# Performance work log

Measured on AMD Instinct MI355X. Metric: run time of the kernel, lower is better.

## Reference

```python
import jax, jax.numpy as jnp
import numpy as np

C = 768; NH = 12; HD = C // NH; P = 16; IMG = 256; HS = IMG // P  # 16x16 patch grid
WIN = 7; HWP = WIN // 2  # half window (pad)
DEPTH = 12; MLP = 4 * C
B = 32; T = 1
OFFS = [(dh, dw) for dh in range(WIN) for dw in range(WIN)]


def ln(x, g, b, eps=1e-5):
    mu = jnp.mean(x, axis=-1, keepdims=True)
    var = jnp.mean((x - mu) ** 2, axis=-1, keepdims=True)
    return (x - mu) * jax.lax.rsqrt(var + eps) * g + b


def local_attn(x, qkv_w, proj_w, proj_b):
    # x: (B, N, C) with N = HS*HS (T=1); sliding-window attention, zero-padded keys
    Bc, N, _ = x.shape
    qkv = (x @ qkv_w.T).reshape(Bc, N, 3, NH, HD)
    q, k, v = [jnp.transpose(qkv[:, :, i], (0, 2, 1, 3)).reshape(Bc, NH, HS, HS, HD)
               for i in range(3)]
    scale = HD ** -0.5
    kp = jnp.pad(k, ((0, 0), (0, 0), (HWP, HWP), (HWP, HWP), (0, 0)))
    vp = jnp.pad(v, ((0, 0), (0, 0), (HWP, HWP), (HWP, HWP), (0, 0)))
    # per-offset logits; padded (zero) keys give logit 0, matching torch's zero-pad softmax
    scores = jnp.stack([
        jnp.einsum('bnhwd,bnhwd->bnhw', q, kp[:, :, dh:dh + HS, dw:dw + HS]) * scale
        for dh, dw in OFFS], axis=-1)  # (B, NH, HS, HS, 49)
    attn = jax.nn.softmax(scores, axis=-1)
    out = sum(attn[..., i, None] * vp[:, :, dh:dh + HS, dw:dw + HS]
              for i, (dh, dw) in enumerate(OFFS))  # (B, NH, HS, HS, HD)
    out = jnp.transpose(out, (0, 2, 3, 1, 4)).reshape(Bc, N, C)
    return out @ proj_w.T + proj_b


def global_attn(x, in_w, in_b, out_w, out_b):
    Bc, N, _ = x.shape
    qkv = x @ in_w.T + in_b
    q, k, v = jnp.split(qkv, 3, axis=-1)
    hds = lambda t: t.reshape(Bc, N, NH, HD).transpose(0, 2, 1, 3)
    q, k, v = hds(q), hds(k), hds(v)
    s = jnp.einsum('bnqd,bnkd->bnqk', q, k) * (HD ** -0.5)
    a = jax.nn.softmax(s, axis=-1)
    o = jnp.einsum('bnqk,bnkd->bnqd', a, v).transpose(0, 2, 1, 3).reshape(Bc, N, C)
    return o @ out_w.T + out_b


def setup_inputs() -> dict:
    key = jax.random.key(0)
    ks = iter(jax.random.split(key, 40))
    s = 0.02
    inp = {
        'x': jax.random.normal(next(ks), (B, T, 3, IMG, IMG), jnp.float32),
        'aspect_ratio': jax.random.uniform(next(ks), (B,), jnp.float32),
        'conv_w': jax.random.normal(next(ks), (C, 3, P, P), jnp.float32) * s,
        'conv_b': jnp.zeros((C,), jnp.float32),
        'pe_g': jnp.ones((C,), jnp.float32), 'pe_b': jnp.zeros((C,), jnp.float32),
        'ar_token': jax.random.normal(next(ks), (1, 1, C), jnp.float32) * s,
        'pos_embed': jax.random.normal(next(ks), (1, 100 * HS * HS + 1, C), jnp.float32) * s,
        'ln1_g': jnp.ones((DEPTH, C), jnp.float32), 'ln1_b': jnp.zeros((DEPTH, C), jnp.float32),
        'ln2_g': jnp.ones((DEPTH, C), jnp.float32), 'ln2_b': jnp.zeros((DEPTH, C), jnp.float32),
        'loc_qkv_w': jax.random.normal(next(ks), (6, 3 * C, C), jnp.float32) * s,
        'loc_proj_w': jax.random.normal(next(ks), (6, C, C), jnp.float32) * s,
        'loc_proj_b': jnp.zeros((6, C), jnp.float32),
        'glob_in_w': jax.random.normal(next(ks), (6, 3 * C, C), jnp.float32) * s,
        'glob_in_b': jnp.zeros((6, 3 * C), jnp.float32),
        'glob_out_w': jax.random.normal(next(ks), (6, C, C), jnp.float32) * s,
        'glob_out_b': jnp.zeros((6, C), jnp.float32),
        'mlp_w1': jax.random.normal(next(ks), (DEPTH, MLP, C), jnp.float32) * s,
        'mlp_b1': jnp.zeros((DEPTH, MLP), jnp.float32),
        'mlp_w2': jax.random.normal(next(ks), (DEPTH, C, MLP), jnp.float32) * s,
        'mlp_b2': jnp.zeros((DEPTH, C), jnp.float32),
        'fin_g': jnp.ones((C,), jnp.float32), 'fin_b': jnp.zeros((C,), jnp.float32),
    }
    return inp


def reference(x, aspect_ratio, conv_w, conv_b, pe_g, pe_b, ar_token, pos_embed,
              ln1_g, ln1_b, ln2_g, ln2_b,
              loc_qkv_w, loc_proj_w, loc_proj_b,
              glob_in_w, glob_in_b, glob_out_w, glob_out_b,
              mlp_w1, mlp_b1, mlp_w2, mlp_b2, fin_g, fin_b):
    Bc, Tc, Ci, Hi, Wi = x.shape
    # patch embed: non-overlapping conv == block reshape + einsum
    xf = x.reshape(Bc * Tc, Ci, HS, P, HS, P)
    patches = jnp.einsum('bchpwq,ecpq->bhwe', xf, conv_w) + conv_b
    patches = patches.reshape(Bc, Tc * HS * HS, C)
    patches = ln(patches, pe_g, pe_b)
    # aspect ratio token
    ar = ar_token * (1.0 + aspect_ratio[:, None, None] * 0.1)  # (B,1,C)
    h = jnp.concatenate([patches, ar], axis=1)
    h = h + pos_embed[:, :h.shape[1], :]
    for i in range(DEPTH):
        if i % 2 == 0:  # local attention block (AR token stripped, N == HS*HS+1)
            li = i // 2
            tok, art = h[:, :-1], h[:, -1:]
            tok = tok + local_attn(ln(tok, ln1_g[i], ln1_b[i]),
                                   loc_qkv_w[li], loc_proj_w[li], loc_proj_b[li])
            h = jnp.concatenate([tok, art], axis=1)
        else:
            gi = i // 2
            h = h + global_attn(ln(h, ln1_g[i], ln1_b[i]),
                                glob_in_w[gi], glob_in_b[gi], glob_out_w[gi], glob_out_b[gi])
        m = ln(h, ln2_g[i], ln2_b[i])
        m = jax.nn.gelu(m @ mlp_w1[i].T + mlp_b1[i], approximate=False)
        h = h + m @ mlp_w2[i].T + mlp_b2[i]
    return ln(h, fin_g, fin_b)
```

## Files before the change

kernel.cpp:

```cpp
#include <hip/hip_runtime.h>
#include <cmath>

#define NHEADS 12
#define NTOK   257
#define BATCH  32
#define ROWS   (BATCH*NTOK)
#define PROWS  (BATCH*256)
#define GTPAD  288

typedef __attribute__((ext_vector_type(8))) short short8;
typedef __attribute__((ext_vector_type(8))) unsigned short u16x8;
typedef __attribute__((ext_vector_type(4))) float f32x4;

__device__ __forceinline__ unsigned short f2bf(float f) {
    unsigned u = __float_as_uint(f);
    unsigned r = (u + 0x7FFFu + ((u >> 16) & 1u)) >> 16;
    return (unsigned short)r;
}
__device__ __forceinline__ float b2f(unsigned short us) {
    return __uint_as_float((unsigned)us << 16);
}
__device__ __forceinline__ void gload16(const void* g, void* l) {
    __builtin_amdgcn_global_load_lds(
        (const __attribute__((address_space(1))) void*)g,
        (__attribute__((address_space(3))) void*)l, 16, 0, 0);
}

template<bool BIAS, bool GELU, bool RES, bool SKIPAR, bool OUTBF>
__global__ __launch_bounds__(256) void gemm_bf16(
    const unsigned short* __restrict__ A, const unsigned short* __restrict__ W,
    const float* __restrict__ bias, void* __restrict__ outv,
    int M, int N, int K)
{
    __shared__ unsigned short As[2][128 * 64];
    __shared__ unsigned short Bs[2][128 * 64];
    const int tid = threadIdx.x;
    const int lane = tid & 63, wid = tid >> 6;
    const int wr = wid >> 1, wc = wid & 1;

    const int gx = gridDim.x;
    const int nwg = gx * gridDim.y;
    const int orig = blockIdx.y * gx + blockIdx.x;
    const int q8 = nwg >> 3, r8 = nwg & 7;
    const int xcd = orig & 7, lid = orig >> 3;
    const int wg = (xcd < r8 ? xcd * (q8 + 1) : r8 * (q8 + 1) + (xcd - r8) * q8) + lid;
    const int bn = (wg % gx) * 128;
    const int bm = (wg / gx) * 128;

    f32x4 acc[4][4];
    #pragma unroll
    for (int i = 0; i < 4; i++)
        #pragma unroll
        for (int j = 0; j < 4; j++) acc[i][j] = (f32x4)0.f;

    const int l15 = lane & 15;
    const int lg  = lane >> 4;
    const int sw  = l15 & 7;

    auto stage = [&](int buf, int k0) {
        #pragma unroll
        for (int it = 0; it < 4; it++) {
            int f = it * 256 + tid;
            int row = f >> 3;
            int g = (f & 3 * 2 + (f & 7) - (f & 7)) ; (void)g;
            int gc = (f & 7) ^ (row & 7);
            gload16(A + (size_t)(bm + row) * K + k0 + gc * 8, &As[buf][f * 8]);
            gload16(W + (size_t)(bn + row) * K + k0 + gc * 8, &Bs[buf][f * 8]);
        }
    };

    const int nt = K >> 6;
    stage(0, 0);
    __syncthreads();

    int buf = 0;
    for (int t = 0; t < nt; t++) {
        if (t + 1 < nt) stage(buf ^ 1, (t + 1) << 6);
        #pragma unroll
        for (int kk = 0; kk < 2; kk++) {
            short8 af[4], bf[4];
            #pragma unroll
            for (int i = 0; i < 4; i++) {
                int row = wr * 64 + i * 16 + l15;
                af[i] = *(const short8*)&As[buf][row * 64 + (((kk * 4 + lg) ^ sw)) * 8];
            }
            #pragma unroll
            for (int j = 0; j < 4; j++) {
                int row = wc * 64 + j * 16 + l15;
                bf[j] = *(const short8*)&Bs[buf][row * 64 + (((kk * 4 + lg) ^ sw)) * 8];
            }
            #pragma unroll
            for (int i = 0; i < 4; i++)
                #pragma unroll
                for (int j = 0; j < 4; j++)
                    acc[i][j] = __builtin_amdgcn_mfma_f32_16x16x32_bf16(af[i], bf[j], acc[i][j], 0, 0, 0);
        }
        __syncthreads();
        buf ^= 1;
    }

    float bcol[4];
    #pragma unroll
    for (int j = 0; j < 4; j++)
        bcol[j] = BIAS ? bias[bn + wc * 64 + j * 16 + l15] : 0.f;

    #pragma unroll
    for (int i = 0; i < 4; i++) {
        #pragma unroll
        for (int r = 0; r < 4; r++) {
            int row = bm + wr * 64 + i * 16 + lg * 4 + r;
            if (row >= M) continue;
            if (SKIPAR && (row % NTOK) == (NTOK - 1)) continue;
            #pragma unroll
            for (int j = 0; j < 4; j++) {
                int col = bn + wc * 64 + j * 16 + l15;
                float v = acc[i][j][r] + bcol[j];
                if (GELU) v = 0.5f * v * (1.0f + erff(v * 0.70710678118654752f));
                size_t idx = (size_t)row * N + col;
                if (OUTBF) {
                    ((unsigned short*)outv)[idx] = f2bf(v);
                } else {
                    float* o = (float*)outv;
                    if (RES) o[idx] += v; else o[idx] = v;
                }
            }
        }
    }
}

template<bool BIAS, bool GELU, bool RES, bool SKIPAR, bool OUTBF>
__global__ __launch_bounds__(512) void gemm256(
    const unsigned short* __restrict__ A, const unsigned short* __restrict__ W,
    const float* __restrict__ bias, void* __restrict__ outv,
    int M, int N, int K)
{
    __shared__ unsigned short As[2][256 * 64];
    __shared__ unsigned short Bs[2][256 * 64];
    const int tid = threadIdx.x;
    const int lane = tid & 63, wid = tid >> 6;
    const int wr = wid >> 2, wc = wid & 3;

    const int gx = gridDim.x;
    const int nwg = gx * gridDim.y;
    const int orig = blockIdx.y * gx + blockIdx.x;
    const int q8 = nwg >> 3, r8 = nwg & 7;
    const int xcd = orig & 7, lid = orig >> 3;
    const int wg = (xcd < r8 ? xcd * (q8 + 1) : r8 * (q8 + 1) + (xcd - r8) * q8) + lid;
    const int bn = (wg % gx) * 256;
    const int bm = (wg / gx) * 256;

    f32x4 acc[8][4];
    #pragma unroll
    for (int i = 0; i < 8; i++)
        #pragma unroll
        for (int j = 0; j < 4; j++) acc[i][j] = (f32x4)0.f;

    const int l15 = lane & 15;
    const int lg  = lane >> 4;
    const int sw  = l15 & 7;

    const int r0 = tid >> 3;
    const int gsrc = (tid & 7) ^ (r0 & 7);
    const int wub = (tid & 448) * 8;

    auto stage = [&](int buf, int k0) {
        #pragma unroll
        for (int it = 0; it < 4; it++) {
            gload16(A + (size_t)(bm + it * 64 + r0) * K + k0 + gsrc * 8,
                    &As[buf][it * 4096 + wub]);
            gload16(W + (size_t)(bn + it * 64 + r0) * K + k0 + gsrc * 8,
                    &Bs[buf][it * 4096 + wub]);
        }
    };

    const int nt = K >> 6;
    stage(0, 0);

    int buf = 0;
    for (int t = 0; t < nt; t++) {
        if (t + 1 < nt) {
            stage(buf ^ 1, (t + 1) << 6);
            asm volatile("s_waitcnt vmcnt(8)\n\ts_barrier" ::: "memory");
        } else {
            asm volatile("s_waitcnt vmcnt(0)\n\ts_barrier" ::: "memory");
        }
        #pragma unroll
        for (int kk = 0; kk < 2; kk++) {
            short8 af[8], bf[4];
            #pragma unroll
            for (int i = 0; i < 8; i++) {
                int row = wr * 128 + i * 16 + l15;
                af[i] = *(const short8*)&As[buf][row * 64 + (((kk * 4 + lg) ^ sw)) * 8];
            }
            #pragma unroll
            for (int j = 0; j < 4; j++) {
                int row = wc * 64 + j * 16 + l15;
                bf[j] = *(const short8*)&Bs[buf][row * 64 + (((kk * 4 + lg) ^ sw)) * 8];
            }
            __builtin_amdgcn_s_setprio(1);
            #pragma unroll
            for (int i = 0; i < 8; i++)
                #pragma unroll
                for (int j = 0; j < 4; j++)
                    acc[i][j] = __builtin_amdgcn_mfma_f32_16x16x32_bf16(af[i], bf[j], acc[i][j], 0, 0, 0);
            __builtin_amdgcn_s_setprio(0);
        }
        asm volatile("s_barrier" ::: "memory");
        buf ^= 1;
    }

    float bcol[4];
    #pragma unroll
    for (int j = 0; j < 4; j++)
        bcol[j] = BIAS ? bias[bn + wc * 64 + j * 16 + l15] : 0.f;

    #pragma unroll
    for (int i = 0; i < 8; i++) {
        #pragma unroll
        for (int r = 0; r < 4; r++) {
            int row = bm + wr * 128 + i * 16 + lg * 4 + r;
            if (row >= M) continue;
            if (SKIPAR && (row % NTOK) == (NTOK - 1)) continue;
            #pragma unroll
            for (int j = 0; j < 4; j++) {
                int col = bn + wc * 64 + j * 16 + l15;
                float v = acc[i][j][r] + bcol[j];
                if (GELU) v = 0.5f * v * (1.0f + erff(v * 0.70710678118654752f));
                size_t idx = (size_t)row * N + col;
                if (OUTBF) {
                    ((unsigned short*)outv)[idx] = f2bf(v);
                } else {
                    float* o = (float*)outv;
                    if (RES) o[idx] += v; else o[idx] = v;
                }
            }
        }
    }
}

template<bool OUTBF>
__global__ __launch_bounds__(256) void ln_kernel(
    const float* __restrict__ in, void* __restrict__ outv,
    const float* __restrict__ g, const float* __restrict__ bparm, int rows)
{
    int gw = blockIdx.x * 4 + (threadIdx.x >> 6);
    int lane = threadIdx.x & 63;
    if (gw >= rows) return;
    const float* x = in + (size_t)gw * 768;
    float4 v[3];
    #pragma unroll
    for (int i = 0; i < 3; i++) v[i] = *(const float4*)(x + i * 256 + lane * 4);
    float s = 0.f;
    #pragma unroll
    for (int i = 0; i < 3; i++) s += v[i].x + v[i].y + v[i].z + v[i].w;
    #pragma unroll
    for (int off = 32; off >= 1; off >>= 1) s += __shfl_xor(s, off, 64);
    float mu = s * (1.f / 768.f);
    float q = 0.f;
    #pragma unroll
    for (int i = 0; i < 3; i++) {
        float dx = v[i].x - mu, dy = v[i].y - mu, dz = v[i].z - mu, dw = v[i].w - mu;
        q += dx * dx + dy * dy + dz * dz + dw * dw;
    }
    #pragma unroll
    for (int off = 32; off >= 1; off >>= 1) q += __shfl_xor(q, off, 64);
    float rstd = rsqrtf(q * (1.f / 768.f) + 1e-5f);
    #pragma unroll
    for (int i = 0; i < 3; i++) {
        float4 gg = *(const float4*)(g + i * 256 + lane * 4);
        float4 bb = *(const float4*)(bparm + i * 256 + lane * 4);
        float rx = (v[i].x - mu) * rstd * gg.x + bb.x;
        float ry = (v[i].y - mu) * rstd * gg.y + bb.y;
        float rz = (v[i].z - mu) * rstd * gg.z + bb.z;
        float rw = (v[i].w - mu) * rstd * gg.w + bb.w;
        if (OUTBF) {
            ushort4 u;
            u.x = f2bf(rx); u.y = f2bf(ry); u.z = f2bf(rz); u.w = f2bf(rw);
            *(ushort4*)((unsigned short*)outv + (size_t)gw * 768 + i * 256 + lane * 4) = u;
        } else {
            *(float4*)((float*)outv + (size_t)gw * 768 + i * 256 + lane * 4) =
                make_float4(rx, ry, rz, rw);
        }
    }
}

__global__ __launch_bounds__(256) void f2b_kernel(
    const float* __restrict__ in, unsigned short* __restrict__ out, int n4)
{
    int i = blockIdx.x * 256 + threadIdx.x;
    if (i >= n4) return;
    float4 v = ((const float4*)in)[i];
    ushort4 u;
    u.x = f2bf(v.x); u.y = f2bf(v.y); u.z = f2bf(v.z); u.w = f2bf(v.w);
    ((ushort4*)out)[i] = u;
}

__global__ __launch_bounds__(256) void gather_patches(
    const float* __restrict__ x, unsigned short* __restrict__ A)
{
    int row = blockIdx.x;
    int b = row >> 8;
    int pp = row & 255;
    int ph = pp >> 4, pw = pp & 15;
    const float* xb = x + (size_t)b * 196608;
    for (int e = threadIdx.x; e < 768; e += 256) {
        int c = e >> 8;
        int r = e & 255;
        int p = r >> 4, q = r & 15;
        A[(size_t)row * 768 + e] = f2bf(xb[(size_t)c * 65536 + (ph * 16 + p) * 256 + pw * 16 + q]);
    }
}

__global__ __launch_bounds__(256) void build_h_kernel(
    const unsigned short* __restrict__ lnp, const float* __restrict__ pos,
    const float* __restrict__ artok, const float* __restrict__ aspect,
    float* __restrict__ h)
{
    int row = blockIdx.x;
    int b = row / NTOK;
    int t = row - b * NTOK;
    float* hp = h + (size_t)row * 768;
    int e = threadIdx.x;
    if (t < 256) {
        const unsigned short* lp = lnp + ((size_t)b * 256 + t) * 768;
        const float* pp = pos + (size_t)t * 768;
        #pragma unroll
        for (int i = 0; i < 3; i++) { int c = e + i * 256; hp[c] = b2f(lp[c]) + pp[c]; }
    } else {
        float f = 1.0f + aspect[b] * 0.1f;
        const float* pp = pos + (size_t)256 * 768;
        #pragma unroll
        for (int i = 0; i < 3; i++) { int c = e + i * 256; hp[c] = artok[c] * f + pp[c]; }
    }
}

__global__ __launch_bounds__(256) void transpose_v(
    const unsigned short* __restrict__ qkv, unsigned short* __restrict__ vt)
{
    __shared__ unsigned short T[64][72];
    const int bh = blockIdx.x;
    const int b = bh / NHEADS, nh = bh % NHEADS;
    const unsigned short* vbase = qkv + (size_t)b * NTOK * 2304 + 1536 + nh * 64;
    unsigned short* obase = vt + (size_t)bh * 64 * GTPAD;
    const int tid = threadIdx.x;

    for (int t0 = 0; t0 < GTPAD; t0 += 64) {
        #pragma unroll
        for (int rnd = 0; rnd < 2; rnd++) {
            int tl = rnd * 32 + (tid >> 3);
            int d0 = (tid & 7) * 8;
            int tok = t0 + tl;
            u16x8 v;
            if (tok < NTOK) {
                v = *(const u16x8*)(vbase + (size_t)tok * 2304 + d0);
            } else {
                #pragma unroll
                for (int i = 0; i < 8; i++) v[i] = 0;
            }
            #pragma unroll
            for (int i = 0; i < 8; i++) T[d0 + i][tl] = v[i];
        }
        __syncthreads();
        int d = tid >> 2, ts = (tid & 3) * 16;
        if (t0 + ts < GTPAD) {
            u16x8 o0, o1;
            #pragma unroll
            for (int i = 0; i < 8; i++) { o0[i] = T[d][ts + i]; o1[i] = T[d][ts + 8 + i]; }
            *(u16x8*)(obase + (size_t)d * GTPAD + t0 + ts) = o0;
            *(u16x8*)(obase + (size_t)d * GTPAD + t0 + ts + 8) = o1;
        }
        __syncthreads();
    }
}

__global__ __launch_bounds__(256) void local_attn_mfma(
    const unsigned short* __restrict__ qkv, const unsigned short* __restrict__ vt,
    unsigned short* __restrict__ out)
{
    __shared__ unsigned short P[4][16 * 136];
    const int wid = threadIdx.x >> 6, lane = threadIdx.x & 63;
    const int gw = blockIdx.x * 4 + wid;
    const int bh = gw >> 4, h0 = gw & 15;
    const int b = bh / NHEADS, nh = bh % NHEADS;
    const int l15 = lane & 15, lg = lane >> 4;
    const unsigned short* base = qkv + (size_t)b * NTOK * 2304 + nh * 64;
    const unsigned short* vtb = vt + (size_t)bh * 64 * GTPAD;
    unsigned short* Pw = P[wid];

    const int qtok = h0 * 16 + l15;
    short8 qf0 = *(const short8*)(base + (size_t)qtok * 2304 + lg * 8);
    short8 qf1 = *(const short8*)(base + (size_t)qtok * 2304 + 32 + lg * 8);

    int r0 = h0 - 3; r0 = r0 < 0 ? 0 : (r0 > 8 ? 8 : r0);

    f32x4 s[8];
    #pragma unroll
    for (int i = 0; i < 8; i++) {
        const unsigned short* kr = base + (size_t)((r0 + i) * 16 + l15) * 2304 + 768;
        short8 kf0 = *(const short8*)(kr + lg * 8);
        short8 kf1 = *(const short8*)(kr + 32 + lg * 8);
        f32x4 z = (f32x4)0.f;
        z = __builtin_amdgcn_mfma_f32_16x16x32_bf16(kf0, qf0, z, 0, 0, 0);
        z = __builtin_amdgcn_mfma_f32_16x16x32_bf16(kf1, qf1, z, 0, 0, 0);
        s[i] = z;
    }

    const int vlo = l15 - 3 < 0 ? 0 : l15 - 3;
    const int vhi = l15 + 3 > 15 ? 15 : l15 + 3;
    const int rlo = h0 - 3 < 0 ? 0 : h0 - 3;
    const int rhi = h0 + 3 > 15 ? 15 : h0 + 3;
    const int n_oob = 49 - (rhi - rlo + 1) * (vhi - vlo + 1);
    float m = n_oob > 0 ? 0.f : -1e30f;
    float sv[32];
    #pragma unroll
    for (int i = 0; i < 8; i++) {
        int kh = r0 + i;
        bool rowok = (kh >= rlo) && (kh <= rhi);
        #pragma unroll
        for (int r = 0; r < 4; r++) {
            int kw = lg * 4 + r;
            bool ok = rowok && (kw >= vlo) && (kw <= vhi);
            float xx = ok ? s[i][r] * 0.125f : -1e30f;
            sv[i * 4 + r] = xx;
            m = fmaxf(m, xx);
        }
    }
    m = fmaxf(m, __shfl_xor(m, 16, 64));
    m = fmaxf(m, __shfl_xor(m, 32, 64));
    float tsum = 0.f;
    #pragma unroll
    for (int i = 0; i < 8; i++) {
        float p0 = __expf(sv[i * 4 + 0] - m);
        float p1 = __expf(sv[i * 4 + 1] - m);
        float p2 = __expf(sv[i * 4 + 2] - m);
        float p3 = __expf(sv[i * 4 + 3] - m);
        tsum += p0 + p1 + p2 + p3;
        unsigned u0 = (unsigned)f2bf(p0) | ((unsigned)f2bf(p1) << 16);
        unsigned u1 = (unsigned)f2bf(p2) | ((unsigned)f2bf(p3) << 16);
        *(uint2*)((char*)Pw + l15 * 272 + i * 32 + lg * 8) = make_uint2(u0, u1);
    }
    tsum += __shfl_xor(tsum, 16, 64);
    tsum += __shfl_xor(tsum, 32, 64);
    float denom = tsum + (float)n_oob * __expf(-m);
    __syncthreads();

    f32x4 acc[4];
    #pragma unroll
    for (int d = 0; d < 4; d++) acc[d] = (f32x4)0.f;
    #pragma unroll
    for (int kt = 0; kt < 128; kt += 32) {
        short8 pf = *(const short8*)((char*)Pw + l15 * 272 + kt * 2 + lg * 16);
        #pragma unroll
        for (int d = 0; d < 4; d++) {
            short8 vf = *(const short8*)(vtb + (size_t)(d * 16 + l15) * GTPAD + r0 * 16 + kt + lg * 8);
            acc[d] = __builtin_amdgcn_mfma_f32_16x16x32_bf16(vf, pf, acc[d], 0, 0, 0);
        }
    }

    float inv = 1.f / denom;
    unsigned short* op = out + ((size_t)b * NTOK + qtok) * 768 + nh * 64;
    #pragma unroll
    for (int d = 0; d < 4; d++) {
        ushort4 o;
        o.x = f2bf(acc[d][0] * inv);
        o.y = f2bf(acc[d][1] * inv);
        o.z = f2bf(acc[d][2] * inv);
        o.w = f2bf(acc[d][3] * inv);
        *(ushort4*)(op + d * 16 + lg * 4) = o;
    }
}

__global__ __launch_bounds__(64) void global_attn_mfma(
    const unsigned short* __restrict__ qkv, const unsigned short* __restrict__ vt,
    unsigned short* __restrict__ out)
{
    __shared__ uint4 Pbuf[80];
    unsigned short* P = (unsigned short*)Pbuf;
    const int blk = blockIdx.x;
    const int bh = blk / 17, qt = blk % 17;
    const int b = bh / NHEADS, nh = bh % NHEADS;
    const int lane = threadIdx.x;
    const int l15 = lane & 15, lg = lane >> 4;
    const unsigned short* base = qkv + (size_t)b * NTOK * 2304 + nh * 64;
    const unsigned short* vtb = vt + (size_t)bh * 64 * GTPAD;

    int qrow = qt * 16 + l15;
    const bool qvalid = qrow < NTOK;
    if (!qvalid) qrow = NTOK - 1;
    short8 qf[2];
    qf[0] = *(const short8*)(base + (size_t)qrow * 2304 + lg * 8);
    qf[1] = *(const short8*)(base + (size_t)qrow * 2304 + 32 + lg * 8);

    f32x4 acc[4];
    #pragma unroll
    for (int i = 0; i < 4; i++) acc[i] = (f32x4)0.f;
    float m = -1e30f, l = 0.f;

    for (int kt = 0; kt < GTPAD; kt += 32) {
        f32x4 s[2];
        #pragma unroll
        for (int hh = 0; hh < 2; hh++) {
            int krow = kt + hh * 16 + l15;
            if (krow > NTOK - 1) krow = NTOK - 1;
            short8 kf0 = *(const short8*)(base + (size_t)krow * 2304 + 768 + lg * 8);
            short8 kf1 = *(const short8*)(base + (size_t)krow * 2304 + 768 + 32 + lg * 8);
            f32x4 z = (f32x4)0.f;
            z = __builtin_amdgcn_mfma_f32_16x16x32_bf16(kf0, qf[0], z, 0, 0, 0);
            z = __builtin_amdgcn_mfma_f32_16x16x32_bf16(kf1, qf[1], z, 0, 0, 0);
            s[hh] = z;
        }
        float sv[8];
        float mt = -1e30f;
        #pragma unroll
        for (int hh = 0; hh < 2; hh++)
            #pragma unroll
            for (int r = 0; r < 4; r++) {
                int key = kt + hh * 16 + lg * 4 + r;
                float v = s[hh][r] * 0.125f;
                if (key >= NTOK) v = -1e30f;
                sv[hh * 4 + r] = v;
                mt = fmaxf(mt, v);
            }
        mt = fmaxf(mt, __shfl_xor(mt, 16, 64));
        mt = fmaxf(mt, __shfl_xor(mt, 32, 64));
        float mn = fmaxf(m, mt);
        float cf = __expf(m - mn);
        float tsum = 0.f;
        unsigned short pb[8];
        #pragma unroll
        for (int i = 0; i < 8; i++) {
            float p = __expf(sv[i] - mn);
            tsum += p;
            pb[i] = f2bf(p);
        }
        tsum += __shfl_xor(tsum, 16, 64);
        tsum += __shfl_xor(tsum, 32, 64);
        l = l * cf + tsum;
        m = mn;
        #pragma unroll
        for (int i = 0; i < 4; i++) acc[i] *= cf;

        unsigned u0 = (unsigned)pb[0] | ((unsigned)pb[1] << 16);
        unsigned u1 = (unsigned)pb[2] | ((unsigned)pb[3] << 16);
        unsigned u2 = (unsigned)pb[4] | ((unsigned)pb[5] << 16);
        unsigned u3 = (unsigned)pb[6] | ((unsigned)pb[7] << 16);
        *(uint2*)((char*)P + l15 * 80 + lg * 8)      = make_uint2(u0, u1);
        *(uint2*)((char*)P + l15 * 80 + 32 + lg * 8) = make_uint2(u2, u3);
        __syncthreads();
        short8 pf = *(const short8*)((char*)P + l15 * 80 + lg * 16);
        #pragma unroll
        for (int d = 0; d < 4; d++) {
            short8 vf = *(const short8*)(vtb + (size_t)(d * 16 + l15) * GTPAD + kt + lg * 8);
            acc[d] = __builtin_amdgcn_mfma_f32_16x16x32_bf16(vf, pf, acc[d], 0, 0, 0);
        }
        __syncthreads();
    }

    if (qvalid) {
        float inv = 1.f / l;
        unsigned short* op = out + ((size_t)b * NTOK + qrow) * 768 + nh * 64;
        #pragma unroll
        for (int d = 0; d < 4; d++) {
            ushort4 o;
            o.x = f2bf(acc[d][0] * inv);
            o.y = f2bf(acc[d][1] * inv);
            o.z = f2bf(acc[d][2] * inv);
            o.w = f2bf(acc[d][3] * inv);
            *(ushort4*)(op + d * 16 + lg * 4) = o;
        }
    }
}

extern "C" void kernel_launch(void* const* d_in, const int* in_sizes, int n_in,
                              void* d_out, int out_size, void* d_ws, size_t ws_size,
                              hipStream_t stream)
{
    const float* x       = (const float*)d_in[0];
    const float* aspect  = (const float*)d_in[1];
    const float* conv_w  = (const float*)d_in[2];
    const float* conv_b  = (const float*)d_in[3];
    const float* pe_g    = (const float*)d_in[4];
    const float* pe_b    = (const float*)d_in[5];
    const float* ar_tok  = (const float*)d_in[6];
    const float* pos     = (const float*)d_in[7];
    const float* ln1_g   = (const float*)d_in[8];
    const float* ln1_b   = (const float*)d_in[9];
    const float* ln2_g   = (const float*)d_in[10];
    const float* ln2_b   = (const float*)d_in[11];
    const float* loc_qkv_w  = (const float*)d_in[12];
    const float* loc_proj_w = (const float*)d_in[13];
    const float* loc_proj_b = (const float*)d_in[14];
    const float* glob_in_w  = (const float*)d_in[15];
    const float* glob_in_b  = (const float*)d_in[16];
    const float* glob_out_w = (const float*)d_in[17];
    const float* glob_out_b = (const float*)d_in[18];
    const float* mlp_w1  = (const float*)d_in[19];
    const float* mlp_b1  = (const float*)d_in[20];
    const float* mlp_w2  = (const float*)d_in[21];
    const float* mlp_b2  = (const float*)d_in[22];
    const float* fin_g   = (const float*)d_in[23];
    const float* fin_b   = (const float*)d_in[24];

    char* w = (char*)d_ws;
    float*          h     = (float*)w;
    unsigned short* lnb   = (unsigned short*)(w + 25264128);
    unsigned short* qkvb  = (unsigned short*)(w + 37896192);
    unsigned short* attnb = (unsigned short*)(w + 75792384);
    unsigned short* mlpb  = (unsigned short*)(w + 88424448);
    float*          pembf = (float*)mlpb;
    unsigned short* vtb   = mlpb;
    char* wp = w + 138952704;
    unsigned short* wconv  = (unsigned short*)wp;               wp += 1179648;
    unsigned short* wlqkv  = (unsigned short*)wp;               wp += 21233664;
    unsigned short* wlproj = (unsigned short*)wp;               wp += 7077888;
    unsigned short* wgin   = (unsigned short*)wp;               wp += 21233664;
    unsigned short* wgout  = (unsigned short*)wp;               wp += 7077888;
    unsigned short* wm1    = (unsigned short*)wp;               wp += 56623104;
    unsigned short* wm2    = (unsigned short*)wp;               wp += 56623104;

    auto cvt = [&](const float* src, unsigned short* dst, int n) {
        int n4 = n / 4;
        f2b_kernel<<<(n4 + 255) / 256, 256, 0, stream>>>(src, dst, n4);
    };
    cvt(conv_w,     wconv,  768 * 768);
    cvt(loc_qkv_w,  wlqkv,  6 * 2304 * 768);
    cvt(loc_proj_w, wlproj, 6 * 768 * 768);
    cvt(glob_in_w,  wgin,   6 * 2304 * 768);
    cvt(glob_out_w, wgout,  6 * 768 * 768);
    cvt(mlp_w1,     wm1,    12 * 3072 * 768);
    cvt(mlp_w2,     wm2,    12 * 768 * 3072);

    gather_patches<<<PROWS, 256, 0, stream>>>(x, qkvb);
    gemm_bf16<true, false, false, false, false><<<dim3(6, 64), 256, 0, stream>>>(
        qkvb, wconv, conv_b, pembf, PROWS, 768, 768);
    ln_kernel<true><<<PROWS / 4, 256, 0, stream>>>(pembf, attnb, pe_g, pe_b, PROWS);
    build_h_kernel<<<ROWS, 256, 0, stream>>>(attnb, pos, ar_tok, aspect, h);

    const int mt = (ROWS + 127) / 128;
    const int mt2 = (ROWS + 255) / 256;
    for (int i = 0; i < 12; i++) {
        int half = i / 2;
        ln_kernel<true><<<(ROWS + 3) / 4, 256, 0, stream>>>(h, lnb, ln1_g + i * 768, ln1_b + i * 768, ROWS);
        if ((i & 1) == 0) {
            gemm_bf16<false, false, false, false, true><<<dim3(18, mt), 256, 0, stream>>>(
                lnb, wlqkv + (size_t)half * 2304 * 768, nullptr, qkvb, ROWS, 2304, 768);
            transpose_v<<<BATCH * NHEADS, 256, 0, stream>>>(qkvb, vtb);
            local_attn_mfma<<<BATCH * NHEADS * 16 / 4, 256, 0, stream>>>(qkvb, vtb, attnb);
            gemm_bf16<true, false, true, true, false><<<dim3(6, mt), 256, 0, stream>>>(
                attnb, wlproj + (size_t)half * 768 * 768, loc_proj_b + half * 768, h, ROWS, 768, 768);
        } else {
            gemm_bf16<true, false, false, false, true><<<dim3(18, mt), 256, 0, stream>>>(
                lnb, wgin + (size_t)half * 2304 * 768, glob_in_b + half * 2304, qkvb, ROWS, 2304, 768);
            transpose_v<<<BATCH * NHEADS, 256, 0, stream>>>(qkvb, vtb);
            global_attn_mfma<<<BATCH * NHEADS * 17, 64, 0, stream>>>(qkvb, vtb, attnb);
            gemm_bf16<true, false, true, false, false><<<dim3(6, mt), 256, 0, stream>>>(
                attnb, wgout + (size_t)half * 768 * 768, glob_out_b + half * 768, h, ROWS, 768, 768);
        }
        ln_kernel<true><<<(ROWS + 3) / 4, 256, 0, stream>>>(h, lnb, ln2_g + i * 768, ln2_b + i * 768, ROWS);
        gemm256<true, true, false, false, true><<<dim3(12, mt2), 512, 0, stream>>>(
            lnb, wm1 + (size_t)i * 3072 * 768, mlp_b1 + i * 3072, mlpb, ROWS, 3072, 768);
        gemm_bf16<true, false, true, false, false><<<dim3(6, mt), 256, 0, stream>>>(
            mlpb, wm2 + (size_t)i * 768 * 3072, mlp_b2 + i * 768, h, ROWS, 768, 3072);
    }
    ln_kernel<false><<<(ROWS + 3) / 4, 256, 0, stream>>>(h, (float*)d_out, fin_g, fin_b, ROWS);
}
```

Before: 3.726 ms.

## Halve gemm256 K-tile to 32 and use tanh-approximate GELU

The 256x256 GEMM now stages 32-wide K slices instead of 64, which halves its LDS footprint and lets it use plain __syncthreads in place of hand-placed waitcnt barriers and setprio. Separately, the exact erf GELU in both GEMM epilogues is replaced by a tanh approximation built on __expf. The smaller K tile doubles the number of barriers per output tile and drops the explicit vmcnt overlap. The GELU swap changes numerics relative to the exact-erf reference.

Result: no change. 3.692 ms (-0.9%).

```diff
diff --git a/kernel.cpp b/kernel.cpp
--- a/kernel.cpp
+++ b/kernel.cpp
@@ -24,6 +24,12 @@
     __builtin_amdgcn_global_load_lds(
         (const __attribute__((address_space(1))) void*)g,
         (__attribute__((address_space(3))) void*)l, 16, 0, 0);
+}
+__device__ __forceinline__ float gelu_f(float x) {
+    float y = 0.7978845608f * (x + 0.044715f * x * x * x);
+    float e = __expf(2.f * y);
+    float t = 1.f - 2.f / (e + 1.f);
+    return 0.5f * x * (1.f + t);
 }
 
 template<bool BIAS, bool GELU, bool RES, bool SKIPAR, bool OUTBF>
@@ -62,7 +68,6 @@
         for (int it = 0; it < 4; it++) {
             int f = it * 256 + tid;
             int row = f >> 3;
-            int g = (f & 3 * 2 + (f & 7) - (f & 7)) ; (void)g;
             int gc = (f & 7) ^ (row & 7);
             gload16(A + (size_t)(bm + row) * K + k0 + gc * 8, &As[buf][f * 8]);
             gload16(W + (size_t)(bn + row) * K + k0 + gc * 8, &Bs[buf][f * 8]);
@@ -115,7 +120,7 @@
             for (int j = 0; j < 4; j++) {
                 int col = bn + wc * 64 + j * 16 + l15;
                 float v = acc[i][j][r] + bcol[j];
-                if (GELU) v = 0.5f * v * (1.0f + erff(v * 0.70710678118654752f));
+                if (GELU) v = gelu_f(v);
                 size_t idx = (size_t)row * N + col;
                 if (OUTBF) {
                     ((unsigned short*)outv)[idx] = f2bf(v);
@@ -134,8 +139,8 @@
     const float* __restrict__ bias, void* __restrict__ outv,
     int M, int N, int K)
 {
-    __shared__ unsigned short As[2][256 * 64];
-    __shared__ unsigned short Bs[2][256 * 64];
+    __shared__ unsigned short As[2][256 * 32];
+    __shared__ unsigned short Bs[2][256 * 32];
     const int tid = threadIdx.x;
     const int lane = tid & 63, wid = tid >> 6;
     const int wr = wid >> 2, wc = wid & 3;
@@ -157,55 +162,43 @@
 
     const int l15 = lane & 15;
     const int lg  = lane >> 4;
-    const int sw  = l15 & 7;
-
-    const int r0 = tid >> 3;
-    const int gsrc = (tid & 7) ^ (r0 & 7);
-    const int wub = (tid & 448) * 8;
+    const int sw3 = l15 & 3;
 
     auto stage = [&](int buf, int k0) {
         #pragma unroll
-        for (int it = 0; it < 4; it++) {
-            gload16(A + (size_t)(bm + it * 64 + r0) * K + k0 + gsrc * 8,
-                    &As[buf][it * 4096 + wub]);
-            gload16(W + (size_t)(bn + it * 64 + r0) * K + k0 + gsrc * 8,
-                    &Bs[buf][it * 4096 + wub]);
+        for (int it = 0; it < 2; it++) {
+            int f = it * 512 + tid;
+            int row = f >> 2;
+            int gc = (f & 3) ^ (row & 3);
+            gload16(A + (size_t)(bm + row) * K + k0 + gc * 8, &As[buf][f * 8]);
+            gload16(W + (size_t)(bn + row) * K + k0 + gc * 8, &Bs[buf][f * 8]);
         }
     };
 
-    const int nt = K >> 6;
+    const int nt = K >> 5;
     stage(0, 0);
+    __syncthreads();
 
     int buf = 0;
     for (int t = 0; t < nt; t++) {
-        if (t + 1 < nt) {
-            stage(buf ^ 1, (t + 1) << 6);
-            asm volatile("s_waitcnt vmcnt(8)\n\ts_barrier" ::: "memory");
-        } else {
-            asm volatile("s_waitcnt vmcnt(0)\n\ts_barrier" ::: "memory");
-        }
-        #pragma unroll
-        for (int kk = 0; kk < 2; kk++) {
-            short8 af[8], bf[4];
-            #pragma unroll
-            for (int i = 0; i < 8; i++) {
-                int row = wr * 128 + i * 16 + l15;
-                af[i] = *(const short8*)&As[buf][row * 64 + (((kk * 4 + lg) ^ sw)) * 8];
-            }
-            #pragma unroll
-            for (int j = 0; j < 4; j++) {
-                int row = wc * 64 + j * 16 + l15;
-                bf[j] = *(const short8*)&Bs[buf][row * 64 + (((kk * 4 + lg) ^ sw)) * 8];
-            }
-            __builtin_amdgcn_s_setprio(1);
-            #pragma unroll
-            for (int i = 0; i < 8; i++)
-                #pragma unroll
-                for (int j = 0; j < 4; j++)
-                    acc[i][j] = __builtin_amdgcn_mfma_f32_16x16x32_bf16(af[i], bf[j], acc[i][j], 0, 0, 0);
-            __builtin_amdgcn_s_setprio(0);
-        }
-        asm volatile("s_barrier" ::: "memory");
+        if (t + 1 < nt) stage(buf ^ 1, (t + 1) << 5);
+        short8 af[8], bf[4];
+        #pragma unroll
+        for (int i = 0; i < 8; i++) {
+            int row = wr * 128 + i * 16 + l15;
+            af[i] = *(const short8*)&As[buf][row * 32 + ((lg ^ sw3)) * 8];
+        }
+        #pragma unroll
+        for (int j = 0; j < 4; j++) {
+            int row = wc * 64 + j * 16 + l15;
+            bf[j] = *(const short8*)&Bs[buf][row * 32 + ((lg ^ sw3)) * 8];
+        }
+        #pragma unroll
+        for (int i = 0; i < 8; i++)
+            #pragma unroll
+            for (int j = 0; j < 4; j++)
+                acc[i][j] = __builtin_amdgcn_mfma_f32_16x16x32_bf16(af[i], bf[j], acc[i][j], 0, 0, 0);
+        __syncthreads();
         buf ^= 1;
     }
 
@@ -225,7 +218,7 @@
             for (int j = 0; j < 4; j++) {
                 int col = bn + wc * 64 + j * 16 + l15;
                 float v = acc[i][j][r] + bcol[j];
-                if (GELU) v = 0.5f * v * (1.0f + erff(v * 0.70710678118654752f));
+                if (GELU) v = gelu_f(v);
                 size_t idx = (size_t)row * N + col;
                 if (OUTBF) {
                     ((unsigned short*)outv)[idx] = f2bf(v);
```
